# Performance work log

Measured on AMD Instinct MI355X. Metric: run time of the kernel, lower is better.

## Reference

```python
import jax, jax.numpy as jnp
import numpy as np

EPS = 1e-5
NUM_HEADS = 8
NUM_GROUPS = 32


def conv1x1(x, w, b):
    # x: [B,C,H,W], w: [O,C], b: [O]
    return jnp.einsum('bchw,oc->bohw', x, w) + b[None, :, None, None]


def group_norm(x, w, b, groups=NUM_GROUPS, eps=EPS):
    B, C, H, W = x.shape
    xg = x.reshape(B, groups, C // groups, H, W)
    mean = xg.mean(axis=(2, 3, 4), keepdims=True)
    var = xg.var(axis=(2, 3, 4), keepdims=True)
    xn = ((xg - mean) * jax.lax.rsqrt(var + eps)).reshape(B, C, H, W)
    return xn * w[None, :, None, None] + b[None, :, None, None]


def setup_inputs() -> dict:
    key = jax.random.key(0)
    ks = jax.random.split(key, 12)
    B, C, H, W = 2, 256, 64, 64
    inner = C  # head_dim * num_heads = 32 * 8
    s = 1.0 / np.sqrt(C)
    return {
        'query_feat': jax.random.normal(ks[0], (B, C, H, W), jnp.float32),
        'key_feat': jax.random.normal(ks[1], (B, C, H, W), jnp.float32),
        'q_w': jax.random.normal(ks[2], (inner, C), jnp.float32) * s,
        'q_b': jnp.zeros((inner,), jnp.float32),
        'k_w': jax.random.normal(ks[3], (inner, C), jnp.float32) * s,
        'k_b': jnp.zeros((inner,), jnp.float32),
        'v_w': jax.random.normal(ks[4], (inner, C), jnp.float32) * s,
        'v_b': jnp.zeros((inner,), jnp.float32),
        'out_w': jax.random.normal(ks[5], (C, inner), jnp.float32) * s,
        'out_b': jnp.zeros((C,), jnp.float32),
        'gn_w': jnp.ones((C,), jnp.float32),
        'gn_b': jnp.zeros((C,), jnp.float32),
    }


def reference(query_feat, key_feat, q_w, q_b, k_w, k_b, v_w, v_b, out_w, out_b, gn_w, gn_b):
    B, C, H, W = query_feat.shape
    N = H * W
    h = NUM_HEADS
    d = C // h
    # 1x1 conv projections, then [B, h, N, d]
    def heads(x):
        return x.reshape(B, h, d, N).transpose(0, 1, 3, 2)
    Q = heads(conv1x1(query_feat, q_w, q_b))
    K = heads(conv1x1(key_feat, k_w, k_b))
    V = heads(conv1x1(key_feat, v_w, v_b))
    scores = jnp.einsum('bhnd,bhmd->bhnm', Q, K) * (d ** -0.5)  # [B,h,N,N]
    attn = jax.nn.softmax(scores, axis=-1)
    out = jnp.einsum('bhnm,bhmd->bhnd', attn, V)  # [B,h,N,d]
    out = out.transpose(0, 1, 3, 2).reshape(B, h * d, H, W)
    proj = conv1x1(out, out_w, out_b)
    return group_norm(query_feat + proj, gn_w, gn_b)
```

## Files before the change

kernel.cpp:

```cpp
#include <hip/hip_runtime.h>
#include <math.h>

#define C_DIM 256
#define N_DIM 4096
#define NHEAD 8

using bf16x8 = __attribute__((ext_vector_type(8))) short;
using f32x16 = __attribute__((ext_vector_type(16))) float;

__device__ __forceinline__ short f32_to_bf16(float a) {
    return (short)((__float_as_uint(a) + 0x8000u) >> 16);
}
__device__ __forceinline__ float bf16_to_f32(unsigned short u) {
    return __uint_as_float(((unsigned)u) << 16);
}
__device__ __forceinline__ unsigned pack_trunc(float a, float b) {
    return __builtin_amdgcn_perm(__float_as_uint(b), __float_as_uint(a), 0x07060302u);
}

__device__ __forceinline__ int SWZ(int m, int c) {
    return (m >> 5) * 8192 + (c >> 4) * 512 + ((c >> 3) & 1) * 256 + (m & 31) * 8 + (c & 7);
}
__device__ __forceinline__ int HS(int i, int d) {
    return (i >> 5) * 1024 + (d >> 4) * 512 + ((d >> 3) & 1) * 256 + (i & 31) * 8 + (d & 7);
}
__device__ __forceinline__ int VS(int d, int k) {
    return (k >> 5) * 1024 + ((k >> 4) & 1) * 512 + ((k >> 3) & 1) * 256 + d * 8 + (k & 7);
}

__global__ __launch_bounds__(256) void prep(
    const float* __restrict__ query, const float* __restrict__ key,
    const float* __restrict__ qw, const float* __restrict__ kw,
    const float* __restrict__ vw, const float* __restrict__ ow,
    short* __restrict__ Qx, short* __restrict__ Kx, short* __restrict__ Wsw)
{
    const int t = threadIdx.x;
    if (blockIdx.z == 4) {
        const int p = blockIdx.y;
        const float* src = (p == 0) ? qw : (p == 1) ? kw : (p == 2) ? vw : ow;
        const int idx = (blockIdx.x * 256 + t) * 4;
        const int o = idx >> 8, c = idx & 255;
        float4 v = *(const float4*)&src[idx];
        short* dst = Wsw + p * 65536 + SWZ(o, c);
        dst[0] = f32_to_bf16(v.x); dst[1] = f32_to_bf16(v.y);
        dst[2] = f32_to_bf16(v.z); dst[3] = f32_to_bf16(v.w);
        return;
    }
    __shared__ short Ts[64][72];
    const int z = blockIdx.z;
    const float* in = (z < 2) ? query : key;
    short* out = ((z < 2) ? Qx : Kx) + (size_t)(z & 1) * N_DIM * C_DIM;
    const size_t ibase = (size_t)(z & 1) * C_DIM * N_DIM;
    const int n0 = blockIdx.x * 64, c0 = blockIdx.y * 64;
    const int cl = t >> 4, nl4 = (t & 15) * 4;
#pragma unroll
    for (int p = 0; p < 4; ++p) {
        const int c = cl + p * 16;
        float4 v = *(const float4*)&in[ibase + (size_t)(c0 + c) * N_DIM + n0 + nl4];
        Ts[nl4 + 0][c] = f32_to_bf16(v.x);
        Ts[nl4 + 1][c] = f32_to_bf16(v.y);
        Ts[nl4 + 2][c] = f32_to_bf16(v.z);
        Ts[nl4 + 3][c] = f32_to_bf16(v.w);
    }
    __syncthreads();
    const int nl = t >> 3, cg = t & 7;
#pragma unroll
    for (int half = 0; half < 2; ++half) {
        const int nloc = nl + half * 32;
        const int c = c0 + cg * 8;
        uint4 val = *(const uint4*)&Ts[nloc][cg * 8];
        *(uint4*)&out[SWZ(n0 + nloc, c)] = val;
    }
}

__global__ __launch_bounds__(256) void qkv_gemm(
    const short* __restrict__ Wsw, const short* __restrict__ Qx,
    const short* __restrict__ Kx,
    const float* __restrict__ q_b, const float* __restrict__ k_b,
    const float* __restrict__ v_b,
    short* __restrict__ Qt, short* __restrict__ Kt, short* __restrict__ Vt,
    float qscale)
{
    const int t = threadIdx.x, w = t >> 6, lane = t & 63;
    const int q2 = lane >> 5, l31 = lane & 31;
    const int proj = blockIdx.z >> 1, b = blockIdx.z & 1;
    const int n0 = blockIdx.x * 64 + (w >> 1) * 32;
    const int o0 = blockIdx.y * 64 + (w & 1) * 32;
    const short* X = ((proj == 0) ? Qx : Kx) + (size_t)b * N_DIM * C_DIM;
    const short* W = Wsw + proj * 65536;
    const float* bias = (proj == 0) ? q_b : (proj == 1) ? k_b : v_b;
    const int xbase = (n0 >> 5) * 8192 + q2 * 256 + l31 * 8;
    const int wbase = (o0 >> 5) * 8192 + q2 * 256 + l31 * 8;

    f32x16 acc;
#pragma unroll
    for (int r = 0; r < 16; ++r) acc[r] = 0.f;

#pragma unroll 4
    for (int kc = 0; kc < C_DIM; kc += 16) {
        bf16x8 xf = *(const bf16x8*)&X[xbase + (kc >> 4) * 512];
        bf16x8 wf = *(const bf16x8*)&W[wbase + (kc >> 4) * 512];
        if (proj == 2)
            acc = __builtin_amdgcn_mfma_f32_32x32x16_bf16(wf, xf, acc, 0, 0, 0);
        else
            acc = __builtin_amdgcn_mfma_f32_32x32x16_bf16(xf, wf, acc, 0, 0, 0);
    }

    const int head = o0 >> 5;
    if (proj < 2) {
        short* OH = ((proj == 0) ? Qt : Kt) + (size_t)(b * NHEAD + head) * N_DIM * 32;
        const float bi = bias[o0 + l31];
        const float sc = (proj == 0) ? qscale : 1.f;
        const int cbase = (n0 >> 5) * 1024 + (l31 >> 4) * 512 + ((l31 >> 3) & 1) * 256 + (l31 & 7);
#pragma unroll
        for (int r = 0; r < 16; ++r) {
            const int qs = (r & 3) + 8 * (r >> 2) + 4 * q2;
            OH[cbase + qs * 8] = f32_to_bf16((acc[r] + bi) * sc);
        }
    } else {
        short* VH = Vt + (size_t)(b * NHEAD + head) * N_DIM * 32;
        const int kbase = (n0 >> 5) * 1024 + (l31 >> 4) * 512 + ((l31 >> 3) & 1) * 256 + (l31 & 7);
#pragma unroll
        for (int r = 0; r < 16; ++r) {
            const int ds = (r & 3) + 8 * (r >> 2) + 4 * q2;
            VH[kbase + ds * 8] = f32_to_bf16(acc[r] + bias[o0 + ds]);
        }
    }
}

__global__ __launch_bounds__(256) void flash_mfma(
    const short* __restrict__ Qt, const short* __restrict__ Kt,
    const short* __restrict__ Vt, short* __restrict__ Opart,
    float* __restrict__ lpart)
{
    const int n0 = blockIdx.x * 128;
    const int h  = blockIdx.y;
    const int z  = blockIdx.z;
    const int b  = z >> 2, s = z & 3;
    const int CHUNK = N_DIM / 4;
    const int t = threadIdx.x, w = t >> 6, lane = t & 63;
    const int q2 = lane >> 5, l31 = lane & 31;
    const int q  = n0 + w * 32 + l31;
    const int bhp = b * NHEAD + h;
    const size_t hb = (size_t)bhp * N_DIM * 32;
    const size_t base = ((size_t)b * C_DIM + (size_t)h * 32) * N_DIM;

    const int qoff = (q >> 5) * 1024 + q2 * 256 + (q & 31) * 8;
    bf16x8 Qf0 = *(const bf16x8*)&Qt[hb + qoff];
    bf16x8 Qf1 = *(const bf16x8*)&Qt[hb + qoff + 512];

    int off = ((s * CHUNK) >> 5) * 1024 + q2 * 256 + l31 * 8;
    bf16x8 Kc0 = *(const bf16x8*)&Kt[hb + off];
    bf16x8 Kc1 = *(const bf16x8*)&Kt[hb + off + 512];
    bf16x8 Vc0 = *(const bf16x8*)&Vt[hb + off];
    bf16x8 Vc1 = *(const bf16x8*)&Vt[hb + off + 512];
    off += 1024;

    f32x16 Of;
#pragma unroll
    for (int r = 0; r < 16; ++r) Of[r] = 0.f;
    float ls = 0.f;

    for (int it = 0; it < CHUNK / 32; ++it) {
        bf16x8 Kn0 = *(const bf16x8*)&Kt[hb + off];
        bf16x8 Kn1 = *(const bf16x8*)&Kt[hb + off + 512];
        bf16x8 Vn0 = *(const bf16x8*)&Vt[hb + off];
        bf16x8 Vn1 = *(const bf16x8*)&Vt[hb + off + 512];
        off += 1024;

        f32x16 acc;
#pragma unroll
        for (int r = 0; r < 16; ++r) acc[r] = 0.f;
        acc = __builtin_amdgcn_mfma_f32_32x32x16_bf16(Kc0, Qf0, acc, 0, 0, 0);
        acc = __builtin_amdgcn_mfma_f32_32x32x16_bf16(Kc1, Qf1, acc, 0, 0, 0);

        float p[16];
#pragma unroll
        for (int r = 0; r < 16; ++r) { p[r] = __builtin_amdgcn_exp2f(acc[r]); ls += p[r]; }

        unsigned u[8], xu[8];
#pragma unroll
        for (int g = 0; g < 8; ++g) u[g] = pack_trunc(p[2 * g], p[2 * g + 1]);
#pragma unroll
        for (int g = 0; g < 8; ++g) xu[g] = (unsigned)__shfl_xor((int)u[g], 32, 64);

        uint4 f0, f1;
        f0.x = q2 ? xu[2] : u[0];  f0.y = q2 ? xu[3] : u[1];
        f0.z = q2 ? u[2]  : xu[0]; f0.w = q2 ? u[3]  : xu[1];
        f1.x = q2 ? xu[6] : u[4];  f1.y = q2 ? xu[7] : u[5];
        f1.z = q2 ? u[6]  : xu[4]; f1.w = q2 ? u[7]  : xu[5];
        bf16x8 Pf0 = __builtin_bit_cast(bf16x8, f0);
        bf16x8 Pf1 = __builtin_bit_cast(bf16x8, f1);

        Of = __builtin_amdgcn_mfma_f32_32x32x16_bf16(Vc0, Pf0, Of, 0, 0, 0);
        Of = __builtin_amdgcn_mfma_f32_32x32x16_bf16(Vc1, Pf1, Of, 0, 0, 0);

        Kc0 = Kn0; Kc1 = Kn1; Vc0 = Vn0; Vc1 = Vn1;
    }

    ls += __shfl_xor(ls, 32, 64);
#pragma unroll
    for (int r = 0; r < 16; ++r) {
        const int d = (r & 3) + 8 * (r >> 2) + 4 * q2;
        Opart[((size_t)(s * 16 + bhp) * 32 + d) * N_DIM + q] = f32_to_bf16(Of[r]);
    }
    lpart[(size_t)(s * 16 + bhp) * N_DIM + q] = ls;
}

__global__ __launch_bounds__(256) void combine4(
    const short* __restrict__ Opart, const float* __restrict__ lpart,
    short* __restrict__ AOt)
{
    const int n0 = blockIdx.x * 64;
    const int p  = blockIdx.y;
    const int bb = p >> 3, hh = p & 7;
    const int t = threadIdx.x;
    __shared__ float linv[64];
    __shared__ short Ts[64][36];

    if (t < 64) {
        float sum = 0.f;
#pragma unroll
        for (int s = 0; s < 4; ++s)
            sum += lpart[(size_t)(s * 16 + p) * N_DIM + n0 + t];
        linv[t] = 1.f / sum;
    }

    const int d  = t >> 3;
    const int n8 = (t & 7) * 8;
    float a[8];
#pragma unroll
    for (int j = 0; j < 8; ++j) a[j] = 0.f;
#pragma unroll
    for (int s = 0; s < 4; ++s) {
        const size_t rb = ((size_t)(s * 16 + p) * 32 + d) * N_DIM + n0 + n8;
        ushort4 u0 = *(const ushort4*)&Opart[rb];
        ushort4 u1 = *(const ushort4*)&Opart[rb + 4];
        a[0] += bf16_to_f32(u0.x); a[1] += bf16_to_f32(u0.y);
        a[2] += bf16_to_f32(u0.z); a[3] += bf16_to_f32(u0.w);
        a[4] += bf16_to_f32(u1.x); a[5] += bf16_to_f32(u1.y);
        a[6] += bf16_to_f32(u1.z); a[7] += bf16_to_f32(u1.w);
    }
    __syncthreads();
#pragma unroll
    for (int j = 0; j < 8; ++j)
        Ts[n8 + j][d] = f32_to_bf16(a[j] * linv[n8 + j]);
    __syncthreads();
    const int dq = (t & 7) * 4;
    const int nr = t >> 3;
#pragma unroll
    for (int p2 = 0; p2 < 2; ++p2) {
        const int n = nr + p2 * 32;
        const int c = hh * 32 + dq;
        ushort4 u = *(const ushort4*)&Ts[n][dq];
        *(ushort4*)&AOt[(size_t)bb * N_DIM * C_DIM + SWZ(n0 + n, c)] = u;
    }
}

__global__ __launch_bounds__(256) void out_gemm(
    const short* __restrict__ OWsw, const short* __restrict__ AOt,
    const float* __restrict__ ob, const float* __restrict__ query,
    float* __restrict__ y)
{
    const int t = threadIdx.x, w = t >> 6, lane = t & 63;
    const int q2 = lane >> 5, l31 = lane & 31;
    const int n0 = blockIdx.x * 32, o0 = blockIdx.y * 32, b = blockIdx.z;
    const short* B = AOt + (size_t)b * N_DIM * C_DIM;
    const int abase = (o0 >> 5) * 8192 + q2 * 256 + l31 * 8;
    const int bbase = (n0 >> 5) * 8192 + q2 * 256 + l31 * 8;

    f32x16 acc;
#pragma unroll
    for (int r = 0; r < 16; ++r) acc[r] = 0.f;

    const int kc0 = w * 64;
#pragma unroll
    for (int s2 = 0; s2 < 4; ++s2) {
        const int kc = kc0 + s2 * 16;
        bf16x8 af = *(const bf16x8*)&OWsw[abase + (kc >> 4) * 512];
        bf16x8 bf = *(const bf16x8*)&B[bbase + (kc >> 4) * 512];
        acc = __builtin_amdgcn_mfma_f32_32x32x16_bf16(af, bf, acc, 0, 0, 0);
    }

    __shared__ float red[3][64][17];
    if (w > 0) {
#pragma unroll
        for (int r = 0; r < 16; ++r) red[w - 1][lane][r] = acc[r];
    }
    __syncthreads();
    if (w == 0) {
#pragma unroll
        for (int r = 0; r < 16; ++r)
            acc[r] += red[0][lane][r] + red[1][lane][r] + red[2][lane][r];
        const size_t base = (size_t)b * C_DIM * N_DIM;
#pragma unroll
        for (int r = 0; r < 16; ++r) {
            const int o = o0 + (r & 3) + 8 * (r >> 2) + 4 * q2;
            const int n = n0 + l31;
            const size_t addr = base + (size_t)o * N_DIM + n;
            y[addr] = acc[r] + ob[o] + query[addr];
        }
    }
}

__global__ __launch_bounds__(256) void groupnorm_kernel(
    float* __restrict__ data, const float* __restrict__ gw,
    const float* __restrict__ gb)
{
    const int g = blockIdx.x;
    const int b = blockIdx.y;
    const size_t base = ((size_t)b * C_DIM + (size_t)g * 8) * N_DIM;
    float4* Y4 = (float4*)(data + base);
    const int t = threadIdx.x;

    float sum = 0.f, sumsq = 0.f;
    for (int i = t; i < 8192; i += 256) {
        float4 v = Y4[i];
        sum   += v.x + v.y + v.z + v.w;
        sumsq += v.x * v.x + v.y * v.y + v.z * v.z + v.w * v.w;
    }
#pragma unroll
    for (int off = 1; off < 64; off <<= 1) {
        sum   += __shfl_xor(sum, off, 64);
        sumsq += __shfl_xor(sumsq, off, 64);
    }
    __shared__ float red[10];
    const int wid = t >> 6;
    if ((t & 63) == 0) { red[wid] = sum; red[4 + wid] = sumsq; }
    __syncthreads();
    if (t == 0) {
        float s = red[0] + red[1] + red[2] + red[3];
        float qq = red[4] + red[5] + red[6] + red[7];
        float mean = s * (1.f / 32768.f);
        float var  = qq * (1.f / 32768.f) - mean * mean;
        red[8] = mean;
        red[9] = rsqrtf(var + 1e-5f);
    }
    __syncthreads();
    const float mean = red[8], rstd = red[9];
    for (int i = t; i < 8192; i += 256) {
        const int c = i >> 10;
        const float wv  = gw[g * 8 + c] * rstd;
        const float bb2 = gb[g * 8 + c];
        float4 v = Y4[i];
        float4 r;
        r.x = (v.x - mean) * wv + bb2;
        r.y = (v.y - mean) * wv + bb2;
        r.z = (v.z - mean) * wv + bb2;
        r.w = (v.w - mean) * wv + bb2;
        Y4[i] = r;
    }
}

extern "C" void kernel_launch(void* const* d_in, const int* in_sizes, int n_in,
                              void* d_out, int out_size, void* d_ws, size_t ws_size,
                              hipStream_t stream)
{
    const float* query = (const float*)d_in[0];
    const float* key   = (const float*)d_in[1];
    const float* q_w   = (const float*)d_in[2];
    const float* q_b   = (const float*)d_in[3];
    const float* k_w   = (const float*)d_in[4];
    const float* k_b   = (const float*)d_in[5];
    const float* v_w   = (const float*)d_in[6];
    const float* v_b   = (const float*)d_in[7];
    const float* o_w   = (const float*)d_in[8];
    const float* o_b   = (const float*)d_in[9];
    const float* gn_w  = (const float*)d_in[10];
    const float* gn_b  = (const float*)d_in[11];

    char* wsb = (char*)d_ws;
    short* Wsw   = (short*)wsb;
    short* Qx    = (short*)(wsb + (1u  << 20));
    short* Kx    = (short*)(wsb + (5u  << 20));
    short* Qt    = (short*)(wsb + (9u  << 20));
    short* Kt    = (short*)(wsb + (13u << 20));
    short* Vt    = (short*)(wsb + (17u << 20));
    short* Opart = (short*)(wsb + (21u << 20));
    float* lpart = (float*)(wsb + (37u << 20));
    short* AOt   = Qx;
    float* y     = (float*)d_out;

    const float qscale = 0.17677669529663687f * 1.4426950408889634f;

    prep<<<dim3(64, 4, 5), 256, 0, stream>>>(query, key, q_w, k_w, v_w, o_w,
                                             Qx, Kx, Wsw);
    qkv_gemm<<<dim3(64, 4, 6), 256, 0, stream>>>(Wsw, Qx, Kx, q_b, k_b, v_b,
                                                 Qt, Kt, Vt, qscale);
    flash_mfma<<<dim3(32, 8, 8), 256, 0, stream>>>(Qt, Kt, Vt, Opart, lpart);
    combine4<<<dim3(64, 16), 256, 0, stream>>>(Opart, lpart, AOt);
    out_gemm<<<dim3(128, 8, 2), 256, 0, stream>>>(Wsw + 3 * 65536, AOt, o_b,
                                                  query, y);
    groupnorm_kernel<<<dim3(32, 2), 256, 0, stream>>>(y, gn_w, gn_b);
}
```

Before: 186.6 us.

## Fuse GroupNorm stats into out_gemm, relayout Opart, and tune flash loop

out_gemm now gives each wave its own 32x32 output tile over the full K dimension. This removes the split-K shared-memory reduction. It also accumulates per-group sum and sum-of-squares, pushed to a workspace buffer with atomics. GroupNorm becomes a pure apply pass over more blocks, so y no longer needs a separate statistics read pass. The flash kernel writes Opart in n-major layout with vector stores, folds the exp into the pack loop with split row-sum accumulators, and unrolls the main loop by two. combine4 drops its LDS transpose as a result. The atomics make the float summation order nondeterministic, and var = E[x²] − mean² in fp32 can lose precision.

```diff
diff --git a/kernel.cpp b/kernel.cpp
--- a/kernel.cpp
+++ b/kernel.cpp
@@ -20,23 +20,19 @@
 
 __device__ __forceinline__ int SWZ(int m, int c) {
     return (m >> 5) * 8192 + (c >> 4) * 512 + ((c >> 3) & 1) * 256 + (m & 31) * 8 + (c & 7);
-}
-__device__ __forceinline__ int HS(int i, int d) {
-    return (i >> 5) * 1024 + (d >> 4) * 512 + ((d >> 3) & 1) * 256 + (i & 31) * 8 + (d & 7);
-}
-__device__ __forceinline__ int VS(int d, int k) {
-    return (k >> 5) * 1024 + ((k >> 4) & 1) * 512 + ((k >> 3) & 1) * 256 + d * 8 + (k & 7);
 }
 
 __global__ __launch_bounds__(256) void prep(
     const float* __restrict__ query, const float* __restrict__ key,
     const float* __restrict__ qw, const float* __restrict__ kw,
     const float* __restrict__ vw, const float* __restrict__ ow,
-    short* __restrict__ Qx, short* __restrict__ Kx, short* __restrict__ Wsw)
+    short* __restrict__ Qx, short* __restrict__ Kx, short* __restrict__ Wsw,
+    float* __restrict__ gstats)
 {
     const int t = threadIdx.x;
     if (blockIdx.z == 4) {
         const int p = blockIdx.y;
+        if (blockIdx.x == 0 && p == 0 && t < 128) gstats[t] = 0.f;
         const float* src = (p == 0) ? qw : (p == 1) ? kw : (p == 2) ? vw : ow;
         const int idx = (blockIdx.x * 256 + t) * 4;
         const int o = idx >> 8, c = idx & 255;
@@ -143,11 +139,12 @@
     const int q  = n0 + w * 32 + l31;
     const int bhp = b * NHEAD + h;
     const size_t hb = (size_t)bhp * N_DIM * 32;
-    const size_t base = ((size_t)b * C_DIM + (size_t)h * 32) * N_DIM;
 
     const int qoff = (q >> 5) * 1024 + q2 * 256 + (q & 31) * 8;
     bf16x8 Qf0 = *(const bf16x8*)&Qt[hb + qoff];
     bf16x8 Qf1 = *(const bf16x8*)&Qt[hb + qoff + 512];
+
+    const f32x16 zc = {};
 
     int off = ((s * CHUNK) >> 5) * 1024 + q2 * 256 + l31 * 8;
     bf16x8 Kc0 = *(const bf16x8*)&Kt[hb + off];
@@ -159,8 +156,9 @@
     f32x16 Of;
 #pragma unroll
     for (int r = 0; r < 16; ++r) Of[r] = 0.f;
-    float ls = 0.f;
-
+    float lsa0 = 0.f, lsa1 = 0.f, lsa2 = 0.f, lsa3 = 0.f;
+
+#pragma unroll 2
     for (int it = 0; it < CHUNK / 32; ++it) {
         bf16x8 Kn0 = *(const bf16x8*)&Kt[hb + off];
         bf16x8 Kn1 = *(const bf16x8*)&Kt[hb + off + 512];
@@ -168,19 +166,20 @@
         bf16x8 Vn1 = *(const bf16x8*)&Vt[hb + off + 512];
         off += 1024;
 
-        f32x16 acc;
-#pragma unroll
-        for (int r = 0; r < 16; ++r) acc[r] = 0.f;
-        acc = __builtin_amdgcn_mfma_f32_32x32x16_bf16(Kc0, Qf0, acc, 0, 0, 0);
+        f32x16 acc = __builtin_amdgcn_mfma_f32_32x32x16_bf16(Kc0, Qf0, zc, 0, 0, 0);
         acc = __builtin_amdgcn_mfma_f32_32x32x16_bf16(Kc1, Qf1, acc, 0, 0, 0);
 
-        float p[16];
-#pragma unroll
-        for (int r = 0; r < 16; ++r) { p[r] = __builtin_amdgcn_exp2f(acc[r]); ls += p[r]; }
-
         unsigned u[8], xu[8];
 #pragma unroll
-        for (int g = 0; g < 8; ++g) u[g] = pack_trunc(p[2 * g], p[2 * g + 1]);
+        for (int g = 0; g < 8; ++g) {
+            float e0 = __builtin_amdgcn_exp2f(acc[2 * g]);
+            float e1 = __builtin_amdgcn_exp2f(acc[2 * g + 1]);
+            u[g] = pack_trunc(e0, e1);
+            if ((g & 3) == 0) lsa0 += e0 + e1;
+            else if ((g & 3) == 1) lsa1 += e0 + e1;
+            else if ((g & 3) == 2) lsa2 += e0 + e1;
+            else lsa3 += e0 + e1;
+        }
 #pragma unroll
         for (int g = 0; g < 8; ++g) xu[g] = (unsigned)__shfl_xor((int)u[g], 32, 64);
 
@@ -198,11 +197,18 @@
         Kc0 = Kn0; Kc1 = Kn1; Vc0 = Vn0; Vc1 = Vn1;
     }
 
+    float ls = (lsa0 + lsa1) + (lsa2 + lsa3);
     ls += __shfl_xor(ls, 32, 64);
-#pragma unroll
-    for (int r = 0; r < 16; ++r) {
-        const int d = (r & 3) + 8 * (r >> 2) + 4 * q2;
-        Opart[((size_t)(s * 16 + bhp) * 32 + d) * N_DIM + q] = f32_to_bf16(Of[r]);
+
+    const size_t obase = ((size_t)(s * 16 + bhp) * N_DIM + q) * 32;
+#pragma unroll
+    for (int g = 0; g < 4; ++g) {
+        ushort4 st;
+        st.x = (unsigned short)f32_to_bf16(Of[4 * g + 0]);
+        st.y = (unsigned short)f32_to_bf16(Of[4 * g + 1]);
+        st.z = (unsigned short)f32_to_bf16(Of[4 * g + 2]);
+        st.w = (unsigned short)f32_to_bf16(Of[4 * g + 3]);
+        *(ushort4*)&Opart[obase + 8 * g + 4 * q2] = st;
     }
     lpart[(size_t)(s * 16 + bhp) * N_DIM + q] = ls;
 }
@@ -216,7 +222,6 @@
     const int bb = p >> 3, hh = p & 7;
     const int t = threadIdx.x;
     __shared__ float linv[64];
-    __shared__ short Ts[64][36];
 
     if (t < 64) {
         float sum = 0.f;
@@ -225,15 +230,16 @@
             sum += lpart[(size_t)(s * 16 + p) * N_DIM + n0 + t];
         linv[t] = 1.f / sum;
     }
-
-    const int d  = t >> 3;
-    const int n8 = (t & 7) * 8;
+    __syncthreads();
+
+    const int nl = t >> 2;
+    const int dg = (t & 3) * 8;
     float a[8];
 #pragma unroll
     for (int j = 0; j < 8; ++j) a[j] = 0.f;
 #pragma unroll
     for (int s = 0; s < 4; ++s) {
-        const size_t rb = ((size_t)(s * 16 + p) * 32 + d) * N_DIM + n0 + n8;
+        const size_t rb = ((size_t)(s * 16 + p) * N_DIM + n0 + nl) * 32 + dg;
         ushort4 u0 = *(const ushort4*)&Opart[rb];
         ushort4 u1 = *(const ushort4*)&Opart[rb + 4];
         a[0] += bf16_to_f32(u0.x); a[1] += bf16_to_f32(u0.y);
@@ -241,30 +247,31 @@
         a[4] += bf16_to_f32(u1.x); a[5] += bf16_to_f32(u1.y);
         a[6] += bf16_to_f32(u1.z); a[7] += bf16_to_f32(u1.w);
     }
-    __syncthreads();
-#pragma unroll
-    for (int j = 0; j < 8; ++j)
-        Ts[n8 + j][d] = f32_to_bf16(a[j] * linv[n8 + j]);
-    __syncthreads();
-    const int dq = (t & 7) * 4;
-    const int nr = t >> 3;
-#pragma unroll
-    for (int p2 = 0; p2 < 2; ++p2) {
-        const int n = nr + p2 * 32;
-        const int c = hh * 32 + dq;
-        ushort4 u = *(const ushort4*)&Ts[n][dq];
-        *(ushort4*)&AOt[(size_t)bb * N_DIM * C_DIM + SWZ(n0 + n, c)] = u;
-    }
+    const float rl = linv[nl];
+    ushort4 o0v, o1v;
+    o0v.x = (unsigned short)f32_to_bf16(a[0] * rl);
+    o0v.y = (unsigned short)f32_to_bf16(a[1] * rl);
+    o0v.z = (unsigned short)f32_to_bf16(a[2] * rl);
+    o0v.w = (unsigned short)f32_to_bf16(a[3] * rl);
+    o1v.x = (unsigned short)f32_to_bf16(a[4] * rl);
+    o1v.y = (unsigned short)f32_to_bf16(a[5] * rl);
+    o1v.z = (unsigned short)f32_to_bf16(a[6] * rl);
+    o1v.w = (unsigned short)f32_to_bf16(a[7] * rl);
+    short* dst = &AOt[(size_t)bb * N_DIM * C_DIM + SWZ(n0 + nl, hh * 32 + dg)];
+    *(ushort4*)dst = o0v;
+    *(ushort4*)(dst + 4) = o1v;
 }
 
 __global__ __launch_bounds__(256) void out_gemm(
     const short* __restrict__ OWsw, const short* __restrict__ AOt,
     const float* __restrict__ ob, const float* __restrict__ query,
-    float* __restrict__ y)
+    float* __restrict__ y, float* __restrict__ gstats)
 {
     const int t = threadIdx.x, w = t >> 6, lane = t & 63;
     const int q2 = lane >> 5, l31 = lane & 31;
-    const int n0 = blockIdx.x * 32, o0 = blockIdx.y * 32, b = blockIdx.z;
+    const int n0 = blockIdx.x * 64 + (w >> 1) * 32;
+    const int o0 = blockIdx.y * 64 + (w & 1) * 32;
+    const int b  = blockIdx.z;
     const short* B = AOt + (size_t)b * N_DIM * C_DIM;
     const int abase = (o0 >> 5) * 8192 + q2 * 256 + l31 * 8;
     const int bbase = (n0 >> 5) * 8192 + q2 * 256 + l31 * 8;
@@ -273,82 +280,71 @@
 #pragma unroll
     for (int r = 0; r < 16; ++r) acc[r] = 0.f;
 
-    const int kc0 = w * 64;
-#pragma unroll
-    for (int s2 = 0; s2 < 4; ++s2) {
-        const int kc = kc0 + s2 * 16;
+#pragma unroll 4
+    for (int kc = 0; kc < C_DIM; kc += 16) {
         bf16x8 af = *(const bf16x8*)&OWsw[abase + (kc >> 4) * 512];
         bf16x8 bf = *(const bf16x8*)&B[bbase + (kc >> 4) * 512];
         acc = __builtin_amdgcn_mfma_f32_32x32x16_bf16(af, bf, acc, 0, 0, 0);
     }
 
-    __shared__ float red[3][64][17];
-    if (w > 0) {
-#pragma unroll
-        for (int r = 0; r < 16; ++r) red[w - 1][lane][r] = acc[r];
-    }
-    __syncthreads();
-    if (w == 0) {
-#pragma unroll
-        for (int r = 0; r < 16; ++r)
-            acc[r] += red[0][lane][r] + red[1][lane][r] + red[2][lane][r];
-        const size_t base = (size_t)b * C_DIM * N_DIM;
-#pragma unroll
-        for (int r = 0; r < 16; ++r) {
-            const int o = o0 + (r & 3) + 8 * (r >> 2) + 4 * q2;
-            const int n = n0 + l31;
-            const size_t addr = base + (size_t)o * N_DIM + n;
-            y[addr] = acc[r] + ob[o] + query[addr];
-        }
-    }
-}
-
-__global__ __launch_bounds__(256) void groupnorm_kernel(
-    float* __restrict__ data, const float* __restrict__ gw,
-    const float* __restrict__ gb)
-{
-    const int g = blockIdx.x;
-    const int b = blockIdx.y;
-    const size_t base = ((size_t)b * C_DIM + (size_t)g * 8) * N_DIM;
-    float4* Y4 = (float4*)(data + base);
+    const size_t base = (size_t)b * C_DIM * N_DIM;
+    float gs[4], gq[4];
+#pragma unroll
+    for (int j = 0; j < 4; ++j) { gs[j] = 0.f; gq[j] = 0.f; }
+#pragma unroll
+    for (int r = 0; r < 16; ++r) {
+        const int o = o0 + (r & 3) + 8 * (r >> 2) + 4 * q2;
+        const int n = n0 + l31;
+        const size_t addr = base + (size_t)o * N_DIM + n;
+        const float v = acc[r] + ob[o] + query[addr];
+        y[addr] = v;
+        gs[r >> 2] += v;
+        gq[r >> 2] += v * v;
+    }
+#pragma unroll
+    for (int offd = 1; offd < 64; offd <<= 1) {
+#pragma unroll
+        for (int j = 0; j < 4; ++j) {
+            gs[j] += __shfl_xor(gs[j], offd, 64);
+            gq[j] += __shfl_xor(gq[j], offd, 64);
+        }
+    }
+    if (lane == 0) {
+#pragma unroll
+        for (int j = 0; j < 4; ++j) {
+            const int grp = b * 32 + (o0 >> 3) + j;
+            atomicAdd(&gstats[grp * 2 + 0], gs[j]);
+            atomicAdd(&gstats[grp * 2 + 1], gq[j]);
+        }
+    }
+}
+
+__global__ __launch_bounds__(256) void gn_apply(
+    float* __restrict__ y, const float* __restrict__ gstats,
+    const float* __restrict__ gw, const float* __restrict__ gb)
+{
+    const int g = blockIdx.x, b = blockIdx.y, sl = blockIdx.z;
+    const float s  = gstats[(b * 32 + g) * 2 + 0];
+    const float qq = gstats[(b * 32 + g) * 2 + 1];
+    const float mean = s * (1.f / 32768.f);
+    const float var  = qq * (1.f / 32768.f) - mean * mean;
+    const float rstd = rsqrtf(var + 1e-5f);
+
+    const size_t base = ((size_t)b * C_DIM + (size_t)g * 8) * N_DIM + sl * 1024;
     const int t = threadIdx.x;
-
-    float sum = 0.f, sumsq = 0.f;
-    for (int i = t; i < 8192; i += 256) {
-        float4 v = Y4[i];
-        sum   += v.x + v.y + v.z + v.w;
-        sumsq += v.x * v.x + v.y * v.y + v.z * v.z + v.w * v.w;
-    }
-#pragma unroll
-    for (int off = 1; off < 64; off <<= 1) {
-        sum   += __shfl_xor(sum, off, 64);
-        sumsq += __shfl_xor(sumsq, off, 64);
-    }
-    __shared__ float red[10];
-    const int wid = t >> 6;
-    if ((t & 63) == 0) { red[wid] = sum; red[4 + wid] = sumsq; }
-    __syncthreads();
-    if (t == 0) {
-        float s = red[0] + red[1] + red[2] + red[3];
-        float qq = red[4] + red[5] + red[6] + red[7];
-        float mean = s * (1.f / 32768.f);
-        float var  = qq * (1.f / 32768.f) - mean * mean;
-        red[8] = mean;
-        red[9] = rsqrtf(var + 1e-5f);
-    }
-    __syncthreads();
-    const float mean = red[8], rstd = red[9];
-    for (int i = t; i < 8192; i += 256) {
-        const int c = i >> 10;
-        const float wv  = gw[g * 8 + c] * rstd;
-        const float bb2 = gb[g * 8 + c];
-        float4 v = Y4[i];
-        float4 r;
-        r.x = (v.x - mean) * wv + bb2;
-        r.y = (v.y - mean) * wv + bb2;
-        r.z = (v.z - mean) * wv + bb2;
-        r.w = (v.w - mean) * wv + bb2;
-        Y4[i] = r;
+#pragma unroll
+    for (int i = 0; i < 8; ++i) {
+        const int idx = t + i * 256;
+        const int row = idx >> 8, col = (idx & 255) * 4;
+        float* ptr = y + base + (size_t)row * N_DIM + col;
+        const float wv  = gw[g * 8 + row] * rstd;
+        const float bb2 = gb[g * 8 + row];
+        float4 v = *(float4*)ptr;
+        v.x = (v.x - mean) * wv + bb2;
+        v.y = (v.y - mean) * wv + bb2;
+        v.z = (v.z - mean) * wv + bb2;
+        v.w = (v.w - mean) * wv + bb2;
+        *(float4*)ptr = v;
     }
 }
 
@@ -371,6 +367,7 @@
 
     char* wsb = (char*)d_ws;
     short* Wsw   = (short*)wsb;
+    float* gstats= (float*)(wsb + (3u << 18));
     short* Qx    = (short*)(wsb + (1u  << 20));
     short* Kx    = (short*)(wsb + (5u  << 20));
     short* Qt    = (short*)(wsb + (9u  << 20));
@@ -384,12 +381,12 @@
     const float qscale = 0.17677669529663687f * 1.4426950408889634f;
 
     prep<<<dim3(64, 4, 5), 256, 0, stream>>>(query, key, q_w, k_w, v_w, o_w,
-                                             Qx, Kx, Wsw);
+                                             Qx, Kx, Wsw, gstats);
     qkv_gemm<<<dim3(64, 4, 6), 256, 0, stream>>>(Wsw, Qx, Kx, q_b, k_b, v_b,
                                                  Qt, Kt, Vt, qscale);
     flash_mfma<<<dim3(32, 8, 8), 256, 0, stream>>>(Qt, Kt, Vt, Opart, lpart);
     combine4<<<dim3(64, 16), 256, 0, stream>>>(Opart, lpart, AOt);
-    out_gemm<<<dim3(128, 8, 2), 256, 0, stream>>>(Wsw + 3 * 65536, AOt, o_b,
-                                                  query, y);
-    groupnorm_kernel<<<dim3(32, 2), 256, 0, stream>>>(y, gn_w, gn_b);
-}
+    out_gemm<<<dim3(64, 4, 2), 256, 0, stream>>>(Wsw + 3 * 65536, AOt, o_b,
+                                                 query, y, gstats);
+    gn_apply<<<dim3(32, 2, 4), 256, 0, stream>>>(y, gstats, gn_w, gn_b);
+}
```

Result: slower. 232.7 us (+24.7%).
